# Optimization experiments

Hardware: AMD Instinct MI355X
Metric: run time of the kernel (lower is better)

## Reference

```python
import jax, jax.numpy as jnp
import numpy as np

B, N, C = 32, 2048, 1024  # batch, tokens, embed_dim
LN_EPS = 1e-5


@jax.custom_vjp
def ste(x):
    # StraightThroughEstimator: hard threshold at 0.5
    return (x > 0.5).astype(x.dtype)

def _ste_fwd(x):
    return ste(x), None

def _ste_bwd(res, g):
    # torch backward: F.hardtanh(grad_output) -> clamp grad to [-1, 1]
    return (jnp.clip(g, -1.0, 1.0),)

ste.defvjp(_ste_fwd, _ste_bwd)


def layernorm(x, scale, bias, eps=LN_EPS):
    mu = jnp.mean(x, axis=-1, keepdims=True)
    var = jnp.mean(jnp.square(x - mu), axis=-1, keepdims=True)
    return (x - mu) * jax.lax.rsqrt(var + eps) * scale + bias


def setup_inputs() -> dict:
    key = jax.random.key(0)
    ks = jax.random.split(key, 8)
    u = lambda k, shape, fan_in: jax.random.uniform(
        k, shape, jnp.float32, -1.0 / np.sqrt(fan_in), 1.0 / np.sqrt(fan_in))
    return {
        "input_feature": jax.random.normal(ks[0], (B, N, C), jnp.float32),
        "noise_feature": jax.random.normal(ks[1], (1, 1, C // 2), jnp.float32),
        "prev_m": jnp.ones((B, N), jnp.float32),
        "ln_scale": jnp.ones((C,), jnp.float32),
        "ln_bias": jnp.zeros((C,), jnp.float32),
        "W_L": u(ks[2], (C, C // 2), C),        # norm1 -> L (no bias)
        "W_l1": u(ks[3], (C, C // 2), C),       # cat(C/2, C/2)=C -> C/2
        "W_l2": u(ks[4], (C // 2, C // 4), C // 2),
        "W_l3": u(ks[5], (C // 4, 1), C // 4),
    }


def reference(input_feature, noise_feature, prev_m,
              ln_scale, ln_bias, W_L, W_l1, W_l2, W_l3):
    Bn, Nn, Cd = input_feature.shape
    # gating MLP (chan_mask_gen)
    h = jax.nn.gelu(layernorm(input_feature, ln_scale, ln_bias) @ W_L,
                    approximate=False)                       # [B,N,C/2]
    nf = jnp.broadcast_to(noise_feature, (Bn, Nn, noise_feature.shape[-1]))
    h = jnp.concatenate([h, nf], axis=-1)                    # [B,N,C]
    h = jax.nn.gelu(h @ W_l1, approximate=False)             # [B,N,C/2]
    h = jax.nn.gelu(h @ W_l2, approximate=False)             # [B,N,C/4]
    prob = jax.nn.sigmoid(h @ W_l3)[..., 0]                  # [B,N]

    # training-path chanFSM: STE mask + elementwise gating
    curr_m = ste(prob * prev_m)                              # {0,1} float
    mask = curr_m.astype(jnp.int32)
    out = input_feature * curr_m[..., None]                  # [B,N,C]
    return out, mask, curr_m + 1e-10
```

## Files before the change

kernel.cpp:

```cpp
#include <hip/hip_runtime.h>
#include <hip/hip_bf16.h>
#include <math.h>

#define T_TOK 65536
#define C_DIM 1024
#define H_DIM 512
#define Q_DIM 256

typedef __attribute__((ext_vector_type(8))) _Float16 half8;
typedef __attribute__((ext_vector_type(4))) float f32x4;
typedef unsigned int u32;
typedef unsigned short u16;

#define MFMAF(a, b, c) __builtin_amdgcn_mfma_f32_16x16x32_f16((a), (b), (c), 0, 0, 0)

#define WS_B1H 0u
#define WS_B1L (WS_B1H + 1048576u)
#define WS_B2H (WS_B1L + 1048576u)
#define WS_B2L (WS_B2H + 524288u)
#define WS_B3H (WS_B2L + 524288u)
#define WS_B3L (WS_B3H + 262144u)
#define WS_BIAS2 (WS_B3L + 262144u)
#define WS_CNT  (WS_BIAS2 + 2048u)
#define WS_LIST (WS_CNT + 256u)
#define WS_W3   (WS_LIST + 32768u)
#define WS_NEED (WS_W3 + 1024u)

#define RC_CAP 8192
#define RC_EPS 5e-5f

__device__ __forceinline__ float gelu_exact(float x) {
    return 0.5f * x * (1.0f + erff(x * 0.70710678118654752440f));
}
__device__ __forceinline__ void split_a(float f, u16& hi, u16& lo) {
    _Float16 h = (_Float16)f;
    _Float16 l = (_Float16)((f - (float)h) * 2048.0f);
    hi = __builtin_bit_cast(u16, h);
    lo = __builtin_bit_cast(u16, l);
}
__device__ __forceinline__ void split_w(float f, u16& hi, u16& lo) {
    _Float16 h = (_Float16)f;
    _Float16 l = (_Float16)(f - (float)h);
    hi = __builtin_bit_cast(u16, h);
    lo = __builtin_bit_cast(u16, l);
}
__device__ __forceinline__ float comb(float m, float r) {
    return fmaf(r, 4.8828125e-4f, m) * 0.03125f;
}

__global__ __launch_bounds__(256) void pack_kernel(const float* __restrict__ WL,
                                                   const float* __restrict__ Wl1,
                                                   const float* __restrict__ Wl2,
                                                   const float* __restrict__ w3,
                                                   unsigned char* __restrict__ ws) {
    u16* B1h = (u16*)(ws + WS_B1H); u16* B1l = (u16*)(ws + WS_B1L);
    u16* B2h = (u16*)(ws + WS_B2H); u16* B2l = (u16*)(ws + WS_B2L);
    u16* B3h = (u16*)(ws + WS_B3H); u16* B3l = (u16*)(ws + WS_B3L);
    int gid = blockIdx.x * 256 + threadIdx.x;
    if (gid == 0) *(int*)(ws + WS_CNT) = 0;
    if (gid < 256) ((float*)(ws + WS_W3))[gid] = w3[gid];
    int lane = gid & 63;
    int tg = gid >> 6;
    int kq = lane >> 4;
    int nn = lane & 15;
    if (tg < 1024) {
        int nt = tg >> 5, kt = tg & 31;
        int n = nt * 16 + nn;
        #pragma unroll
        for (int j = 0; j < 8; ++j) {
            int k = kt * 32 + kq * 8 + j;
            u16 h, l; split_w(WL[(size_t)k * 512 + n] * 32.0f, h, l);
            B1h[(size_t)tg * 512 + lane * 8 + j] = h;
            B1l[(size_t)tg * 512 + lane * 8 + j] = l;
        }
    } else if (tg < 1536) {
        int t2 = tg - 1024;
        int nt = t2 >> 4, kt = t2 & 15;
        int n = nt * 16 + nn;
        #pragma unroll
        for (int j = 0; j < 8; ++j) {
            int k = kt * 32 + kq * 8 + j;
            u16 h, l; split_w(Wl1[(size_t)k * 512 + n] * 32.0f, h, l);
            B2h[(size_t)t2 * 512 + lane * 8 + j] = h;
            B2l[(size_t)t2 * 512 + lane * 8 + j] = l;
        }
    } else if (tg < 1792) {
        int t3 = tg - 1536;
        int nt = t3 >> 4, kt = t3 & 15;
        int n = nt * 16 + nn;
        #pragma unroll
        for (int j = 0; j < 8; ++j) {
            int k = kt * 32 + kq * 8 + j;
            u16 h, l; split_w(Wl2[(size_t)k * 256 + n] * 32.0f, h, l);
            B3h[(size_t)t3 * 512 + lane * 8 + j] = h;
            B3l[(size_t)t3 * 512 + lane * 8 + j] = l;
        }
    }
}

__global__ void bias2_kernel(const float* __restrict__ nf,
                             const float* __restrict__ Wl1,
                             float* __restrict__ bias2) {
    int n = blockIdx.x * blockDim.x + threadIdx.x;
    if (n >= H_DIM) return;
    float s = 0.0f;
    for (int j = 0; j < H_DIM; ++j)
        s = fmaf(nf[j], Wl1[(size_t)(H_DIM + j) * H_DIM + n], s);
    bias2[n] = s;
}

#define MTOK 32
#define SA_STR 136
#define SH_STR 520
#define S3_STR 260

__global__ __launch_bounds__(512, 4)
void chanFSM_mfma_kernel(const float* __restrict__ x,
                         const float* __restrict__ prev_m,
                         const float* __restrict__ gamma,
                         const float* __restrict__ beta,
                         const unsigned char* __restrict__ ws,
                         float* __restrict__ out,
                         float* __restrict__ out_mask,
                         float* __restrict__ out_curr) {
    __shared__ __align__(16) unsigned char smem[66560];
    __shared__ float sMu[MTOK], sRs[MTOK], sFlag[MTOK];
    __shared__ float sBias[H_DIM];
    __shared__ float sw3[Q_DIM];

    u16* sAh = (u16*)smem;
    u16* sAl = sAh + MTOK * SA_STR;
    u16* sHh = (u16*)smem;
    u16* sHl = sHh + MTOK * SH_STR;
    float* sH3 = (float*)smem;

    const u16* B1h = (const u16*)(ws + WS_B1H); const u16* B1l = (const u16*)(ws + WS_B1L);
    const u16* B2h = (const u16*)(ws + WS_B2H); const u16* B2l = (const u16*)(ws + WS_B2L);
    const u16* B3h = (const u16*)(ws + WS_B3H); const u16* B3l = (const u16*)(ws + WS_B3L);
    int* rc_cnt  = (int*)(ws + WS_CNT);
    int* rc_list = (int*)(ws + WS_LIST);

    const int tid = threadIdx.x;
    const int t0  = blockIdx.x * MTOK;
    const int wid = tid >> 6;
    const int ln  = tid & 63;
    const int rg  = wid & 1;
    const int cg  = wid >> 1;
    const int lm  = ln & 15;
    const int lq  = ln >> 4;

    if (tid < H_DIM) sBias[tid] = ((const float*)(ws + WS_BIAS2))[tid];
    if (tid < Q_DIM) sw3[tid] = ((const float*)(ws + WS_W3))[tid];

    for (int m = wid * 4; m < wid * 4 + 4; ++m) {
        const float* row = x + (size_t)(t0 + m) * C_DIM;
        double ds = 0.0, dq = 0.0;
        #pragma unroll
        for (int j = 0; j < 16; ++j) {
            float v = row[ln + (j << 6)];
            ds += (double)v; dq += (double)v * (double)v;
        }
        #pragma unroll
        for (int off = 32; off > 0; off >>= 1) {
            ds += __shfl_down(ds, off);
            dq += __shfl_down(dq, off);
        }
        if (ln == 0) {
            double mu = ds * (1.0 / 1024.0);
            double var = dq * (1.0 / 1024.0) - mu * mu;
            sMu[m] = (float)mu;
            sRs[m] = 1.0f / sqrtf((float)var + 1e-5f);
        }
    }

    f32x4 acc_m[8], acc_r[8];
    #pragma unroll
    for (int c = 0; c < 8; ++c) {
        acc_m[c] = (f32x4){0.f, 0.f, 0.f, 0.f};
        acc_r[c] = (f32x4){0.f, 0.f, 0.f, 0.f};
    }

    for (int chunk = 0; chunk < 8; ++chunk) {
        __syncthreads();
        #pragma unroll
        for (int i = 0; i < 2; ++i) {
            int fq = tid + (i << 9);
            int row = fq >> 5, kq = fq & 31;
            const float4 v = *(const float4*)&x[(size_t)(t0 + row) * C_DIM + chunk * 128 + kq * 4];
            float mu = sMu[row], rs = sRs[row];
            int gk = chunk * 128 + kq * 4;
            float a0 = fmaf((v.x - mu) * rs, gamma[gk],     beta[gk]);
            float a1 = fmaf((v.y - mu) * rs, gamma[gk + 1], beta[gk + 1]);
            float a2 = fmaf((v.z - mu) * rs, gamma[gk + 2], beta[gk + 2]);
            float a3 = fmaf((v.w - mu) * rs, gamma[gk + 3], beta[gk + 3]);
            u16 h0, l0, h1, l1, h2, l2, h3, l3;
            split_a(a0, h0, l0); split_a(a1, h1, l1);
            split_a(a2, h2, l2); split_a(a3, h3, l3);
            uint2 ph = make_uint2((u32)h0 | ((u32)h1 << 16), (u32)h2 | ((u32)h3 << 16));
            uint2 pl = make_uint2((u32)l0 | ((u32)l1 << 16), (u32)l2 | ((u32)l3 << 16));
            *(uint2*)&sAh[row * SA_STR + kq * 4] = ph;
            *(uint2*)&sAl[row * SA_STR + kq * 4] = pl;
        }
        __syncthreads();

        #pragma unroll
        for (int kt = 0; kt < 4; ++kt) {
            int row = rg * 16 + lm;
            half8 ah = *(const half8*)&sAh[row * SA_STR + kt * 32 + lq * 8];
            half8 al = *(const half8*)&sAl[row * SA_STR + kt * 32 + lq * 8];
            int ktg = chunk * 4 + kt;
            #pragma unroll
            for (int chf = 0; chf < 2; ++chf) {
                half8 bh[4], bl[4];
                #pragma unroll
                for (int c = 0; c < 4; ++c) {
                    int tile = (cg * 8 + chf * 4 + c) * 32 + ktg;
                    bh[c] = *(const half8*)&B1h[(size_t)tile * 512 + ln * 8];
                    bl[c] = *(const half8*)&B1l[(size_t)tile * 512 + ln * 8];
                }
                #pragma unroll
                for (int c = 0; c < 4; ++c) {
                    int cc = chf * 4 + c;
                    acc_m[cc] = MFMAF(ah, bh[c], acc_m[cc]);
                    acc_m[cc] = MFMAF(ah, bl[c], acc_m[cc]);
                    acc_r[cc] = MFMAF(al, bh[c], acc_r[cc]);
                }
            }
        }
    }
    __syncthreads();
    #pragma unroll
    for (int c = 0; c < 8; ++c) {
        int col = (cg * 8 + c) * 16 + lm;
        #pragma unroll
        for (int r = 0; r < 4; ++r) {
            int row = rg * 16 + lq * 4 + r;
            u16 h, l; split_a(gelu_exact(comb(acc_m[c][r], acc_r[c][r])), h, l);
            sHh[row * SH_STR + col] = h;
            sHl[row * SH_STR + col] = l;
        }
    }
    __syncthreads();

    f32x4 acc2_m[8], acc2_r[8];
    #pragma unroll
    for (int c = 0; c < 8; ++c) {
        float b = sBias[(cg * 8 + c) * 16 + lm] * 32.0f;
        acc2_m[c] = (f32x4){b, b, b, b};
        acc2_r[c] = (f32x4){0.f, 0.f, 0.f, 0.f};
    }
    #pragma unroll 2
    for (int kt = 0; kt < 16; ++kt) {
        int row = rg * 16 + lm;
        half8 ah = *(const half8*)&sHh[row * SH_STR + kt * 32 + lq * 8];
        half8 al = *(const half8*)&sHl[row * SH_STR + kt * 32 + lq * 8];
        #pragma unroll
        for (int chf = 0; chf < 2; ++chf) {
            half8 bh[4], bl[4];
            #pragma unroll
            for (int c = 0; c < 4; ++c) {
                int tile = (cg * 8 + chf * 4 + c) * 16 + kt;
                bh[c] = *(const half8*)&B2h[(size_t)tile * 512 + ln * 8];
                bl[c] = *(const half8*)&B2l[(size_t)tile * 512 + ln * 8];
            }
            #pragma unroll
            for (int c = 0; c < 4; ++c) {
                int cc = chf * 4 + c;
                acc2_m[cc] = MFMAF(ah, bh[c], acc2_m[cc]);
                acc2_m[cc] = MFMAF(ah, bl[c], acc2_m[cc]);
                acc2_r[cc] = MFMAF(al, bh[c], acc2_r[cc]);
            }
        }
    }
    __syncthreads();
    #pragma unroll
    for (int c = 0; c < 8; ++c) {
        int col = (cg * 8 + c) * 16 + lm;
        #pragma unroll
        for (int r = 0; r < 4; ++r) {
            int row = rg * 16 + lq * 4 + r;
            u16 h, l; split_a(gelu_exact(comb(acc2_m[c][r], acc2_r[c][r])), h, l);
            sHh[row * SH_STR + col] = h;
            sHl[row * SH_STR + col] = l;
        }
    }
    __syncthreads();

    f32x4 acc3_m[4], acc3_r[4];
    #pragma unroll
    for (int c = 0; c < 4; ++c) {
        acc3_m[c] = (f32x4){0.f, 0.f, 0.f, 0.f};
        acc3_r[c] = (f32x4){0.f, 0.f, 0.f, 0.f};
    }
    #pragma unroll 2
    for (int kt = 0; kt < 16; ++kt) {
        int row = rg * 16 + lm;
        half8 ah = *(const half8*)&sHh[row * SH_STR + kt * 32 + lq * 8];
        half8 al = *(const half8*)&sHl[row * SH_STR + kt * 32 + lq * 8];
        half8 bh[4], bl[4];
        #pragma unroll
        for (int c = 0; c < 4; ++c) {
            int tile = (cg * 4 + c) * 16 + kt;
            bh[c] = *(const half8*)&B3h[(size_t)tile * 512 + ln * 8];
            bl[c] = *(const half8*)&B3l[(size_t)tile * 512 + ln * 8];
        }
        #pragma unroll
        for (int c = 0; c < 4; ++c) {
            acc3_m[c] = MFMAF(ah, bh[c], acc3_m[c]);
            acc3_m[c] = MFMAF(ah, bl[c], acc3_m[c]);
            acc3_r[c] = MFMAF(al, bh[c], acc3_r[c]);
        }
    }
    __syncthreads();
    #pragma unroll
    for (int c = 0; c < 4; ++c) {
        int col = (cg * 4 + c) * 16 + lm;
        #pragma unroll
        for (int r = 0; r < 4; ++r) {
            int row = rg * 16 + lq * 4 + r;
            sH3[row * S3_STR + col] = gelu_exact(comb(acc3_m[c][r], acc3_r[c][r]));
        }
    }
    __syncthreads();

    for (int m = wid * 4; m < wid * 4 + 4; ++m) {
        float z = 0.0f;
        #pragma unroll
        for (int j = 0; j < 4; ++j) {
            int k = ln + (j << 6);
            z = fmaf(sH3[m * S3_STR + k], sw3[k], z);
        }
        #pragma unroll
        for (int off = 32; off > 0; off >>= 1) z += __shfl_down(z, off);
        if (ln == 0) {
            float prob = 1.0f / (1.0f + expf(-z));
            float t = prob * prev_m[t0 + m];
            float c = (t > 0.5f) ? 1.0f : 0.0f;
            sFlag[m] = c;
            out_mask[t0 + m] = c;
            out_curr[t0 + m] = (c > 0.0f) ? 1.0f : 1e-10f;
            if (fabsf(t - 0.5f) < RC_EPS) {
                int i = atomicAdd(rc_cnt, 1);
                if (i < RC_CAP) rc_list[i] = t0 + m;
            }
        }
    }
    __syncthreads();

    const float4* x4 = (const float4*)(x   + (size_t)t0 * C_DIM);
    float4*       o4 = (float4*)      (out + (size_t)t0 * C_DIM);
    #pragma unroll 4
    for (int i = 0; i < 16; ++i) {
        int idx = tid + (i << 9);
        int m = idx >> 8;
        float c = sFlag[m];
        float4 v = x4[idx];
        v.x *= c; v.y *= c; v.z *= c; v.w *= c;
        o4[idx] = v;
    }
}

__global__ __launch_bounds__(256, 2)
void recheck_kernel(const float* __restrict__ x, const float* __restrict__ prev_m,
                    const float* __restrict__ gamma, const float* __restrict__ beta,
                    const float* __restrict__ WL, const float* __restrict__ Wl1,
                    const float* __restrict__ Wl2, const float* __restrict__ w3,
                    const unsigned char* __restrict__ ws,
                    float* __restrict__ out, float* __restrict__ out_mask,
                    float* __restrict__ out_curr) {
    __shared__ __align__(16) float sx[8 * 1024];
    __shared__ __align__(16) float sh1[8 * 512];
    __shared__ __align__(16) float sh2[8 * 512];
    __shared__ __align__(16) float sh3[8 * 256];
    __shared__ double srA[8][4], srB[8][4];
    __shared__ float sMu[8], sRs[8], sFlag[8];
    __shared__ int sTok[8];

    const float* bias2 = (const float*)(ws + WS_BIAS2);
    const int* cnt = (const int*)(ws + WS_CNT);
    const int* list = (const int*)(ws + WS_LIST);
    int n = *cnt; if (n > RC_CAP) n = RC_CAP;
    if (blockIdx.x * 8 >= n) return;

    const int tid = threadIdx.x, wid = tid >> 6, ln = tid & 63;

    if (tid < 8) {
        int it = blockIdx.x * 8 + tid;
        sTok[tid] = (it < n) ? list[it] : -1;
    }
    __syncthreads();

    #pragma unroll
    for (int g = 0; g < 8; ++g) {
        int tk = sTok[g];
        if (tk >= 0) {
            const float* row = x + (size_t)tk * C_DIM;
            #pragma unroll
            for (int j = 0; j < 4; ++j)
                sx[g * 1024 + tid + (j << 8)] = row[tid + (j << 8)];
        } else {
            #pragma unroll
            for (int j = 0; j < 4; ++j)
                sx[g * 1024 + tid + (j << 8)] = 0.f;
        }
    }
    __syncthreads();

    #pragma unroll
    for (int g = 0; g < 8; ++g) {
        double ds = 0.0, dq = 0.0;
        #pragma unroll
        for (int j = 0; j < 4; ++j) {
            float v = sx[g * 1024 + tid + (j << 8)];
            ds += (double)v; dq += (double)v * (double)v;
        }
        #pragma unroll
        for (int off = 32; off > 0; off >>= 1) {
            ds += __shfl_down(ds, off); dq += __shfl_down(dq, off);
        }
        if (ln == 0) { srA[g][wid] = ds; srB[g][wid] = dq; }
    }
    __syncthreads();
    if (tid < 8) {
        double tds = srA[tid][0] + srA[tid][1] + srA[tid][2] + srA[tid][3];
        double tdq = srB[tid][0] + srB[tid][1] + srB[tid][2] + srB[tid][3];
        double mud = tds * (1.0 / 1024.0);
        sMu[tid] = (float)mud;
        sRs[tid] = 1.0f / sqrtf((float)(tdq * (1.0 / 1024.0) - mud * mud) + 1e-5f);
    }
    __syncthreads();
    #pragma unroll
    for (int g = 0; g < 8; ++g) {
        float mu = sMu[g], rs = sRs[g];
        #pragma unroll
        for (int j = 0; j < 4; ++j) {
            int k = tid + (j << 8);
            sx[g * 1024 + k] = fmaf((sx[g * 1024 + k] - mu) * rs, gamma[k], beta[k]);
        }
    }
    __syncthreads();

    {
        float acc[2][8][4];
        #pragma unroll
        for (int o = 0; o < 2; ++o)
            #pragma unroll
            for (int g = 0; g < 8; ++g)
                #pragma unroll
                for (int i = 0; i < 4; ++i) acc[o][g][i] = 0.f;
        const float2* Wp = (const float2*)WL + tid;
        #pragma unroll 4
        for (int k = 0; k < 1024; k += 4) {
            float2 w0 = Wp[(size_t)(k + 0) * 256];
            float2 w1 = Wp[(size_t)(k + 1) * 256];
            float2 w2 = Wp[(size_t)(k + 2) * 256];
            float2 w3v = Wp[(size_t)(k + 3) * 256];
            #pragma unroll
            for (int g = 0; g < 8; ++g) {
                float4 a = *(const float4*)&sx[g * 1024 + k];
                acc[0][g][0] = fmaf(a.x, w0.x, acc[0][g][0]);
                acc[1][g][0] = fmaf(a.x, w0.y, acc[1][g][0]);
                acc[0][g][1] = fmaf(a.y, w1.x, acc[0][g][1]);
                acc[1][g][1] = fmaf(a.y, w1.y, acc[1][g][1]);
                acc[0][g][2] = fmaf(a.z, w2.x, acc[0][g][2]);
                acc[1][g][2] = fmaf(a.z, w2.y, acc[1][g][2]);
                acc[0][g][3] = fmaf(a.w, w3v.x, acc[0][g][3]);
                acc[1][g][3] = fmaf(a.w, w3v.y, acc[1][g][3]);
            }
        }
        #pragma unroll
        for (int g = 0; g < 8; ++g) {
            float o0 = (acc[0][g][0] + acc[0][g][1]) + (acc[0][g][2] + acc[0][g][3]);
            float o1 = (acc[1][g][0] + acc[1][g][1]) + (acc[1][g][2] + acc[1][g][3]);
            float2 gv; gv.x = gelu_exact(o0); gv.y = gelu_exact(o1);
            *(float2*)&sh1[g * 512 + 2 * tid] = gv;
        }
    }
    __syncthreads();

    {
        float acc[2][8][4];
        float2 b2 = ((const float2*)bias2)[tid];
        #pragma unroll
        for (int g = 0; g < 8; ++g) {
            acc[0][g][0] = b2.x; acc[1][g][0] = b2.y;
            #pragma unroll
            for (int i = 1; i < 4; ++i) { acc[0][g][i] = 0.f; acc[1][g][i] = 0.f; }
        }
        const float2* Wp = (const float2*)Wl1 + tid;
        #pragma unroll 4
        for (int k = 0; k < 512; k += 4) {
            float2 w0 = Wp[(size_t)(k + 0) * 256];
            float2 w1 = Wp[(size_t)(k + 1) * 256];
            float2 w2 = Wp[(size_t)(k + 2) * 256];
            float2 w3v = Wp[(size_t)(k + 3) * 256];
            #pragma unroll
            for (int g = 0; g < 8; ++g) {
                float4 a = *(const float4*)&sh1[g * 512 + k];
                acc[0][g][0] = fmaf(a.x, w0.x, acc[0][g][0]);
                acc[1][g][0] = fmaf(a.x, w0.y, acc[1][g][0]);
                acc[0][g][1] = fmaf(a.y, w1.x, acc[0][g][1]);
                acc[1][g][1] = fmaf(a.y, w1.y, acc[1][g][1]);
                acc[0][g][2] = fmaf(a.z, w2.x, acc[0][g][2]);
                acc[1][g][2] = fmaf(a.z, w2.y, acc[1][g][2]);
                acc[0][g][3] = fmaf(a.w, w3v.x, acc[0][g][3]);
                acc[1][g][3] = fmaf(a.w, w3v.y, acc[1][g][3]);
            }
        }
        #pragma unroll
        for (int g = 0; g < 8; ++g) {
            float o0 = (acc[0][g][0] + acc[0][g][1]) + (acc[0][g][2] + acc[0][g][3]);
            float o1 = (acc[1][g][0] + acc[1][g][1]) + (acc[1][g][2] + acc[1][g][3]);
            float2 gv; gv.x = gelu_exact(o0); gv.y = gelu_exact(o1);
            *(float2*)&sh2[g * 512 + 2 * tid] = gv;
        }
    }
    __syncthreads();

    {
        float acc[8][4];
        #pragma unroll
        for (int g = 0; g < 8; ++g)
            #pragma unroll
            for (int i = 0; i < 4; ++i) acc[g][i] = 0.f;
        const float* Wp = Wl2 + tid;
        #pragma unroll 4
        for (int k = 0; k < 512; k += 4) {
            float w0 = Wp[(size_t)(k + 0) * 256];
            float w1 = Wp[(size_t)(k + 1) * 256];
            float w2 = Wp[(size_t)(k + 2) * 256];
            float w3v = Wp[(size_t)(k + 3) * 256];
            #pragma unroll
            for (int g = 0; g < 8; ++g) {
                float4 a = *(const float4*)&sh2[g * 512 + k];
                acc[g][0] = fmaf(a.x, w0, acc[g][0]);
                acc[g][1] = fmaf(a.y, w1, acc[g][1]);
                acc[g][2] = fmaf(a.z, w2, acc[g][2]);
                acc[g][3] = fmaf(a.w, w3v, acc[g][3]);
            }
        }
        #pragma unroll
        for (int g = 0; g < 8; ++g)
            sh3[g * 256 + tid] = gelu_exact((acc[g][0] + acc[g][1]) + (acc[g][2] + acc[g][3]));
    }
    __syncthreads();

    {
        float zz[8];
        float wv = w3[tid];
        #pragma unroll
        for (int g = 0; g < 8; ++g) zz[g] = sh3[g * 256 + tid] * wv;
        #pragma unroll
        for (int off = 32; off > 0; off >>= 1) {
            #pragma unroll
            for (int g = 0; g < 8; ++g) zz[g] += __shfl_down(zz[g], off);
        }
        if (ln == 0) {
            #pragma unroll
            for (int g = 0; g < 8; ++g) srA[g][wid] = (double)zz[g];
        }
    }
    __syncthreads();
    if (tid < 8) {
        int tk = sTok[tid];
        if (tk >= 0) {
            float z = (float)(srA[tid][0] + srA[tid][1] + srA[tid][2] + srA[tid][3]);
            float prob = 1.0f / (1.0f + expf(-z));
            float t = prob * prev_m[tk];
            float c = (t > 0.5f) ? 1.0f : 0.0f;
            out_mask[tk] = c;
            out_curr[tk] = (c > 0.0f) ? 1.0f : 1e-10f;
            sFlag[tid] = c;
        }
    }
    __syncthreads();
    #pragma unroll
    for (int g = 0; g < 8; ++g) {
        int tk = sTok[g];
        if (tk < 0) continue;
        float c = sFlag[g];
        float4 v = ((const float4*)(x + (size_t)tk * C_DIM))[tid];
        v.x *= c; v.y *= c; v.z *= c; v.w *= c;
        ((float4*)(out + (size_t)tk * C_DIM))[tid] = v;
    }
}

extern "C" void kernel_launch(void* const* d_in, const int* in_sizes, int n_in,
                              void* d_out, int out_size, void* d_ws, size_t ws_size,
                              hipStream_t stream) {
    const float* x      = (const float*)d_in[0];
    const float* nf     = (const float*)d_in[1];
    const float* prev_m = (const float*)d_in[2];
    const float* gamma  = (const float*)d_in[3];
    const float* beta   = (const float*)d_in[4];
    const float* WL     = (const float*)d_in[5];
    const float* Wl1    = (const float*)d_in[6];
    const float* Wl2    = (const float*)d_in[7];
    const float* w3     = (const float*)d_in[8];

    float* out      = (float*)d_out;
    float* out_mask = out + (size_t)T_TOK * C_DIM;
    float* out_curr = out_mask + T_TOK;

    unsigned char* ws = (unsigned char*)d_ws;

    pack_kernel<<<448, 256, 0, stream>>>(WL, Wl1, Wl2, w3, ws);
    bias2_kernel<<<1, 512, 0, stream>>>(nf, Wl1, (float*)(ws + WS_BIAS2));

    chanFSM_mfma_kernel<<<T_TOK / MTOK, 512, 0, stream>>>(
        x, prev_m, gamma, beta, ws, out, out_mask, out_curr);

    recheck_kernel<<<RC_CAP / 8, 256, 0, stream>>>(
        x, prev_m, gamma, beta, WL, Wl1, Wl2, w3, ws, out, out_mask, out_curr);
}
```

Baseline: 1.726 ms.

## Double tile rows per block, double-buffer LN staging, widen recheck kernel

The main MLP kernel now handles 64 tokens per block, with each wave computing two 16-row MFMA tiles, so every weight fragment loaded from global memory is reused twice. The LayerNorm-to-fp16 staging is double-buffered: the next chunk of x is loaded into registers and written to the other LDS buffer while the current one is consumed, which removes one barrier per chunk. The recheck kernel moves to 512 threads processing 16 tokens per block. The cost is roughly doubled LDS use (133KB) and accumulator registers, with launch bounds lowered to 2 blocks, so occupancy and latency hiding may drop.

Result: slower. 1.832 ms (+6.1%).

```diff
diff --git a/kernel.cpp b/kernel.cpp
--- a/kernel.cpp
+++ b/kernel.cpp
@@ -104,17 +104,45 @@
     int n = blockIdx.x * blockDim.x + threadIdx.x;
     if (n >= H_DIM) return;
     float s = 0.0f;
+    #pragma unroll 8
     for (int j = 0; j < H_DIM; ++j)
         s = fmaf(nf[j], Wl1[(size_t)(H_DIM + j) * H_DIM + n], s);
     bias2[n] = s;
 }
 
-#define MTOK 32
+#define MTOK 64
 #define SA_STR 136
 #define SH_STR 520
 #define S3_STR 260
 
-__global__ __launch_bounds__(512, 4)
+__device__ __forceinline__ void stage_proc(u16* __restrict__ dAh, u16* __restrict__ dAl,
+                                           const float4* xv, int tid, int chunk,
+                                           const float* __restrict__ sMu,
+                                           const float* __restrict__ sRs,
+                                           const float* __restrict__ gamma,
+                                           const float* __restrict__ beta) {
+    #pragma unroll
+    for (int i = 0; i < 4; ++i) {
+        int fq = tid + (i << 9);
+        int row = fq >> 5, kq = fq & 31;
+        float mu = sMu[row], rs = sRs[row];
+        int gk = chunk * 128 + kq * 4;
+        float4 v = xv[i];
+        float a0 = fmaf((v.x - mu) * rs, gamma[gk],     beta[gk]);
+        float a1 = fmaf((v.y - mu) * rs, gamma[gk + 1], beta[gk + 1]);
+        float a2 = fmaf((v.z - mu) * rs, gamma[gk + 2], beta[gk + 2]);
+        float a3 = fmaf((v.w - mu) * rs, gamma[gk + 3], beta[gk + 3]);
+        u16 h0, l0, h1, l1, h2, l2, h3, l3;
+        split_a(a0, h0, l0); split_a(a1, h1, l1);
+        split_a(a2, h2, l2); split_a(a3, h3, l3);
+        uint2 ph = make_uint2((u32)h0 | ((u32)h1 << 16), (u32)h2 | ((u32)h3 << 16));
+        uint2 pl = make_uint2((u32)l0 | ((u32)l1 << 16), (u32)l2 | ((u32)l3 << 16));
+        *(uint2*)&dAh[row * SA_STR + kq * 4] = ph;
+        *(uint2*)&dAl[row * SA_STR + kq * 4] = pl;
+    }
+}
+
+__global__ __launch_bounds__(512, 2)
 void chanFSM_mfma_kernel(const float* __restrict__ x,
                          const float* __restrict__ prev_m,
                          const float* __restrict__ gamma,
@@ -123,13 +151,16 @@
                          float* __restrict__ out,
                          float* __restrict__ out_mask,
                          float* __restrict__ out_curr) {
-    __shared__ __align__(16) unsigned char smem[66560];
+    __shared__ __align__(16) unsigned char smem[133120];
     __shared__ float sMu[MTOK], sRs[MTOK], sFlag[MTOK];
     __shared__ float sBias[H_DIM];
     __shared__ float sw3[Q_DIM];
 
-    u16* sAh = (u16*)smem;
-    u16* sAl = sAh + MTOK * SA_STR;
+    u16* sA[4];
+    sA[0] = (u16*)smem;
+    sA[1] = sA[0] + MTOK * SA_STR;
+    sA[2] = sA[1] + MTOK * SA_STR;
+    sA[3] = sA[2] + MTOK * SA_STR;
     u16* sHh = (u16*)smem;
     u16* sHl = sHh + MTOK * SH_STR;
     float* sH3 = (float*)smem;
@@ -152,7 +183,7 @@
     if (tid < H_DIM) sBias[tid] = ((const float*)(ws + WS_BIAS2))[tid];
     if (tid < Q_DIM) sw3[tid] = ((const float*)(ws + WS_W3))[tid];
 
-    for (int m = wid * 4; m < wid * 4 + 4; ++m) {
+    for (int m = wid * 8; m < wid * 8 + 8; ++m) {
         const float* row = x + (size_t)(t0 + m) * C_DIM;
         double ds = 0.0, dq = 0.0;
         #pragma unroll
@@ -173,42 +204,48 @@
         }
     }
 
-    f32x4 acc_m[8], acc_r[8];
-    #pragma unroll
-    for (int c = 0; c < 8; ++c) {
-        acc_m[c] = (f32x4){0.f, 0.f, 0.f, 0.f};
-        acc_r[c] = (f32x4){0.f, 0.f, 0.f, 0.f};
-    }
-
-    for (int chunk = 0; chunk < 8; ++chunk) {
+    f32x4 acc_m[2][8], acc_r[2][8];
+    #pragma unroll
+    for (int rt = 0; rt < 2; ++rt)
+        #pragma unroll
+        for (int c = 0; c < 8; ++c) {
+            acc_m[rt][c] = (f32x4){0.f, 0.f, 0.f, 0.f};
+            acc_r[rt][c] = (f32x4){0.f, 0.f, 0.f, 0.f};
+        }
+
+    float4 xv[4];
+    #pragma unroll
+    for (int i = 0; i < 4; ++i) {
+        int fq = tid + (i << 9);
+        int row = fq >> 5, kq = fq & 31;
+        xv[i] = *(const float4*)&x[(size_t)(t0 + row) * C_DIM + kq * 4];
+    }
+    __syncthreads();
+    stage_proc(sA[0], sA[1], xv, tid, 0, sMu, sRs, gamma, beta);
+
+    for (int ch = 0; ch < 8; ++ch) {
+        if (ch < 7) {
+            #pragma unroll
+            for (int i = 0; i < 4; ++i) {
+                int fq = tid + (i << 9);
+                int row = fq >> 5, kq = fq & 31;
+                xv[i] = *(const float4*)&x[(size_t)(t0 + row) * C_DIM + (ch + 1) * 128 + kq * 4];
+            }
+        }
         __syncthreads();
-        #pragma unroll
-        for (int i = 0; i < 2; ++i) {
-            int fq = tid + (i << 9);
-            int row = fq >> 5, kq = fq & 31;
-            const float4 v = *(const float4*)&x[(size_t)(t0 + row) * C_DIM + chunk * 128 + kq * 4];
-            float mu = sMu[row], rs = sRs[row];
-            int gk = chunk * 128 + kq * 4;
-            float a0 = fmaf((v.x - mu) * rs, gamma[gk],     beta[gk]);
-            float a1 = fmaf((v.y - mu) * rs, gamma[gk + 1], beta[gk + 1]);
-            float a2 = fmaf((v.z - mu) * rs, gamma[gk + 2], beta[gk + 2]);
-            float a3 = fmaf((v.w - mu) * rs, gamma[gk + 3], beta[gk + 3]);
-            u16 h0, l0, h1, l1, h2, l2, h3, l3;
-            split_a(a0, h0, l0); split_a(a1, h1, l1);
-            split_a(a2, h2, l2); split_a(a3, h3, l3);
-            uint2 ph = make_uint2((u32)h0 | ((u32)h1 << 16), (u32)h2 | ((u32)h3 << 16));
-            uint2 pl = make_uint2((u32)l0 | ((u32)l1 << 16), (u32)l2 | ((u32)l3 << 16));
-            *(uint2*)&sAh[row * SA_STR + kq * 4] = ph;
-            *(uint2*)&sAl[row * SA_STR + kq * 4] = pl;
-        }
-        __syncthreads();
+        const u16* pAh = sA[(ch & 1) * 2];
+        const u16* pAl = sA[(ch & 1) * 2 + 1];
 
         #pragma unroll
         for (int kt = 0; kt < 4; ++kt) {
-            int row = rg * 16 + lm;
-            half8 ah = *(const half8*)&sAh[row * SA_STR + kt * 32 + lq * 8];
-            half8 al = *(const half8*)&sAl[row * SA_STR + kt * 32 + lq * 8];
-            int ktg = chunk * 4 + kt;
+            half8 ah[2], al[2];
+            #pragma unroll
+            for (int rt = 0; rt < 2; ++rt) {
+                int row = rg * 32 + rt * 16 + lm;
+                ah[rt] = *(const half8*)&pAh[row * SA_STR + kt * 32 + lq * 8];
+                al[rt] = *(const half8*)&pAl[row * SA_STR + kt * 32 + lq * 8];
+            }
+            int ktg = ch * 4 + kt;
             #pragma unroll
             for (int chf = 0; chf < 2; ++chf) {
                 half8 bh[4], bl[4];
@@ -219,41 +256,54 @@
                     bl[c] = *(const half8*)&B1l[(size_t)tile * 512 + ln * 8];
                 }
                 #pragma unroll
-                for (int c = 0; c < 4; ++c) {
-                    int cc = chf * 4 + c;
-                    acc_m[cc] = MFMAF(ah, bh[c], acc_m[cc]);
-                    acc_m[cc] = MFMAF(ah, bl[c], acc_m[cc]);
-                    acc_r[cc] = MFMAF(al, bh[c], acc_r[cc]);
-                }
-            }
-        }
-    }
-    __syncthreads();
-    #pragma unroll
-    for (int c = 0; c < 8; ++c) {
-        int col = (cg * 8 + c) * 16 + lm;
-        #pragma unroll
-        for (int r = 0; r < 4; ++r) {
-            int row = rg * 16 + lq * 4 + r;
-            u16 h, l; split_a(gelu_exact(comb(acc_m[c][r], acc_r[c][r])), h, l);
-            sHh[row * SH_STR + col] = h;
-            sHl[row * SH_STR + col] = l;
-        }
-    }
-    __syncthreads();
-
-    f32x4 acc2_m[8], acc2_r[8];
-    #pragma unroll
-    for (int c = 0; c < 8; ++c) {
-        float b = sBias[(cg * 8 + c) * 16 + lm] * 32.0f;
-        acc2_m[c] = (f32x4){b, b, b, b};
-        acc2_r[c] = (f32x4){0.f, 0.f, 0.f, 0.f};
-    }
+                for (int c = 0; c < 4; ++c)
+                    #pragma unroll
+                    for (int rt = 0; rt < 2; ++rt) {
+                        int cc = chf * 4 + c;
+                        acc_m[rt][cc] = MFMAF(ah[rt], bh[c], acc_m[rt][cc]);
+                        acc_m[rt][cc] = MFMAF(ah[rt], bl[c], acc_m[rt][cc]);
+                        acc_r[rt][cc] = MFMAF(al[rt], bh[c], acc_r[rt][cc]);
+                    }
+            }
+        }
+        if (ch < 7)
+            stage_proc(sA[((ch + 1) & 1) * 2], sA[((ch + 1) & 1) * 2 + 1],
+                       xv, tid, ch + 1, sMu, sRs, gamma, beta);
+    }
+    __syncthreads();
+    #pragma unroll
+    for (int rt = 0; rt < 2; ++rt)
+        #pragma unroll
+        for (int c = 0; c < 8; ++c) {
+            int col = (cg * 8 + c) * 16 + lm;
+            #pragma unroll
+            for (int r = 0; r < 4; ++r) {
+                int row = rg * 32 + rt * 16 + lq * 4 + r;
+                u16 h, l; split_a(gelu_exact(comb(acc_m[rt][c][r], acc_r[rt][c][r])), h, l);
+                sHh[row * SH_STR + col] = h;
+                sHl[row * SH_STR + col] = l;
+            }
+        }
+    __syncthreads();
+
+    f32x4 acc2_m[2][8], acc2_r[2][8];
+    #pragma unroll
+    for (int rt = 0; rt < 2; ++rt)
+        #pragma unroll
+        for (int c = 0; c < 8; ++c) {
+            float b = sBias[(cg * 8 + c) * 16 + lm] * 32.0f;
+            acc2_m[rt][c] = (f32x4){b, b, b, b};
+            acc2_r[rt][c] = (f32x4){0.f, 0.f, 0.f, 0.f};
+        }
     #pragma unroll 2
     for (int kt = 0; kt < 16; ++kt) {
-        int row = rg * 16 + lm;
-        half8 ah = *(const half8*)&sHh[row * SH_STR + kt * 32 + lq * 8];
-        half8 al = *(const half8*)&sHl[row * SH_STR + kt * 32 + lq * 8];
+        half8 ah[2], al[2];
+        #pragma unroll
+        for (int rt = 0; rt < 2; ++rt) {
+            int row = rg * 32 + rt * 16 + lm;
+            ah[rt] = *(const half8*)&sHh[row * SH_STR + kt * 32 + lq * 8];
+            al[rt] = *(const half8*)&sHl[row * SH_STR + kt * 32 + lq * 8];
+        }
         #pragma unroll
         for (int chf = 0; chf < 2; ++chf) {
             half8 bh[4], bl[4];
@@ -264,39 +314,49 @@
                 bl[c] = *(const half8*)&B2l[(size_t)tile * 512 + ln * 8];
             }
             #pragma unroll
-            for (int c = 0; c < 4; ++c) {
-                int cc = chf * 4 + c;
-                acc2_m[cc] = MFMAF(ah, bh[c], acc2_m[cc]);
-                acc2_m[cc] = MFMAF(ah, bl[c], acc2_m[cc]);
-                acc2_r[cc] = MFMAF(al, bh[c], acc2_r[cc]);
-            }
-        }
-    }
-    __syncthreads();
-    #pragma unroll
-    for (int c = 0; c < 8; ++c) {
-        int col = (cg * 8 + c) * 16 + lm;
-        #pragma unroll
-        for (int r = 0; r < 4; ++r) {
-            int row = rg * 16 + lq * 4 + r;
-            u16 h, l; split_a(gelu_exact(comb(acc2_m[c][r], acc2_r[c][r])), h, l);
-            sHh[row * SH_STR + col] = h;
-            sHl[row * SH_STR + col] = l;
-        }
-    }
-    __syncthreads();
-
-    f32x4 acc3_m[4], acc3_r[4];
-    #pragma unroll
-    for (int c = 0; c < 4; ++c) {
-        acc3_m[c] = (f32x4){0.f, 0.f, 0.f, 0.f};
-        acc3_r[c] = (f32x4){0.f, 0.f, 0.f, 0.f};
-    }
+            for (int c = 0; c < 4; ++c)
+                #pragma unroll
+                for (int rt = 0; rt < 2; ++rt) {
+                    int cc = chf * 4 + c;
+                    acc2_m[rt][cc] = MFMAF(ah[rt], bh[c], acc2_m[rt][cc]);
+                    acc2_m[rt][cc] = MFMAF(ah[rt], bl[c], acc2_m[rt][cc]);
+                    acc2_r[rt][cc] = MFMAF(al[rt], bh[c], acc2_r[rt][cc]);
+                }
+        }
+    }
+    __syncthreads();
+    #pragma unroll
+    for (int rt = 0; rt < 2; ++rt)
+        #pragma unroll
+        for (int c = 0; c < 8; ++c) {
+            int col = (cg * 8 + c) * 16 + lm;
+            #pragma unroll
+            for (int r = 0; r < 4; ++r) {
+                int row = rg * 32 + rt * 16 + lq * 4 + r;
+                u16 h, l; split_a(gelu_exact(comb(acc2_m[rt][c][r], acc2_r[rt][c][r])), h, l);
+                sHh[row * SH_STR + col] = h;
+                sHl[row * SH_STR + col] = l;
+            }
+        }
+    __syncthreads();
+
+    f32x4 acc3_m[2][4], acc3_r[2][4];
+    #pragma unroll
+    for (int rt = 0; rt < 2; ++rt)
+        #pragma unroll
+        for (int c = 0; c < 4; ++c) {
+            acc3_m[rt][c] = (f32x4){0.f, 0.f, 0.f, 0.f};
+            acc3_r[rt][c] = (f32x4){0.f, 0.f, 0.f, 0.f};
+        }
     #pragma unroll 2
     for (int kt = 0; kt < 16; ++kt) {
-        int row = rg * 16 + lm;
-        half8 ah = *(const half8*)&sHh[row * SH_STR + kt * 32 + lq * 8];
-        half8 al = *(const half8*)&sHl[row * SH_STR + kt * 32 + lq * 8];
+        half8 ah[2], al[2];
+        #pragma unroll
+        for (int rt = 0; rt < 2; ++rt) {
+            int row = rg * 32 + rt * 16 + lm;
+            ah[rt] = *(const half8*)&sHh[row * SH_STR + kt * 32 + lq * 8];
+            al[rt] = *(const half8*)&sHl[row * SH_STR + kt * 32 + lq * 8];
+        }
         half8 bh[4], bl[4];
         #pragma unroll
         for (int c = 0; c < 4; ++c) {
@@ -305,25 +365,29 @@
             bl[c] = *(const half8*)&B3l[(size_t)tile * 512 + ln * 8];
         }
         #pragma unroll
+        for (int c = 0; c < 4; ++c)
+            #pragma unroll
+            for (int rt = 0; rt < 2; ++rt) {
+                acc3_m[rt][c] = MFMAF(ah[rt], bh[c], acc3_m[rt][c]);
+                acc3_m[rt][c] = MFMAF(ah[rt], bl[c], acc3_m[rt][c]);
+                acc3_r[rt][c] = MFMAF(al[rt], bh[c], acc3_r[rt][c]);
+            }
+    }
+    __syncthreads();
+    #pragma unroll
+    for (int rt = 0; rt < 2; ++rt)
+        #pragma unroll
         for (int c = 0; c < 4; ++c) {
-            acc3_m[c] = MFMAF(ah, bh[c], acc3_m[c]);
-            acc3_m[c] = MFMAF(ah, bl[c], acc3_m[c]);
-            acc3_r[c] = MFMAF(al, bh[c], acc3_r[c]);
-        }
-    }
-    __syncthreads();
-    #pragma unroll
-    for (int c = 0; c < 4; ++c) {
-        int col = (cg * 4 + c) * 16 + lm;
-        #pragma unroll
-        for (int r = 0; r < 4; ++r) {
-            int row = rg * 16 + lq * 4 + r;
-            sH3[row * S3_STR + col] = gelu_exact(comb(acc3_m[c][r], acc3_r[c][r]));
-        }
-    }
-    __syncthreads();
-
-    for (int m = wid * 4; m < wid * 4 + 4; ++m) {
+            int col = (cg * 4 + c) * 16 + lm;
+            #pragma unroll
+            for (int r = 0; r < 4; ++r) {
+                int row = rg * 32 + rt * 16 + lq * 4 + r;
+                sH3[row * S3_STR + col] = gelu_exact(comb(acc3_m[rt][c][r], acc3_r[rt][c][r]));
+            }
+        }
+    __syncthreads();
+
+    for (int m = wid * 8; m < wid * 8 + 8; ++m) {
         float z = 0.0f;
         #pragma unroll
         for (int j = 0; j < 4; ++j) {
@@ -350,7 +414,7 @@
     const float4* x4 = (const float4*)(x   + (size_t)t0 * C_DIM);
     float4*       o4 = (float4*)      (out + (size_t)t0 * C_DIM);
     #pragma unroll 4
-    for (int i = 0; i < 16; ++i) {
+    for (int i = 0; i < 32; ++i) {
         int idx = tid + (i << 9);
         int m = idx >> 8;
         float c = sFlag[m];
@@ -360,7 +424,7 @@
     }
 }
 
-__global__ __launch_bounds__(256, 2)
+__global__ __launch_bounds__(512)
 void recheck_kernel(const float* __restrict__ x, const float* __restrict__ prev_m,
                     const float* __restrict__ gamma, const float* __restrict__ beta,
                     const float* __restrict__ WL, const float* __restrict__ Wl1,
@@ -368,60 +432,63 @@
                     const unsigned char* __restrict__ ws,
                     float* __restrict__ out, float* __restrict__ out_mask,
                     float* __restrict__ out_curr) {
-    __shared__ __align__(16) float sx[8 * 1024];
-    __shared__ __align__(16) float sh1[8 * 512];
-    __shared__ __align__(16) float sh2[8 * 512];
-    __shared__ __align__(16) float sh3[8 * 256];
-    __shared__ double srA[8][4], srB[8][4];
-    __shared__ float sMu[8], sRs[8], sFlag[8];
-    __shared__ int sTok[8];
+    __shared__ __align__(16) float sx[16 * 1024];
+    __shared__ __align__(16) float sh1[16 * 512];
+    __shared__ __align__(16) float sh2[16 * 512];
+    __shared__ __align__(16) float sh3[16 * 256];
+    __shared__ double srA[16][4], srB[16][4];
+    __shared__ float sMu[16], sRs[16], sFlag[16];
+    __shared__ int sTok[16];
 
     const float* bias2 = (const float*)(ws + WS_BIAS2);
     const int* cnt = (const int*)(ws + WS_CNT);
     const int* list = (const int*)(ws + WS_LIST);
     int n = *cnt; if (n > RC_CAP) n = RC_CAP;
-    if (blockIdx.x * 8 >= n) return;
-
-    const int tid = threadIdx.x, wid = tid >> 6, ln = tid & 63;
-
-    if (tid < 8) {
-        int it = blockIdx.x * 8 + tid;
+    if (blockIdx.x * 16 >= n) return;
+
+    const int tid = threadIdx.x;
+    const int grp = tid >> 8;
+    const int t8  = tid & 255;
+    const int wid8 = t8 >> 6;
+    const int ln  = tid & 63;
+
+    if (tid < 16) {
+        int it = blockIdx.x * 16 + tid;
         sTok[tid] = (it < n) ? list[it] : -1;
     }
     __syncthreads();
 
     #pragma unroll
-    for (int g = 0; g < 8; ++g) {
+    for (int g = 0; g < 16; ++g) {
         int tk = sTok[g];
         if (tk >= 0) {
             const float* row = x + (size_t)tk * C_DIM;
-            #pragma unroll
-            for (int j = 0; j < 4; ++j)
-                sx[g * 1024 + tid + (j << 8)] = row[tid + (j << 8)];
+            sx[g * 1024 + tid]       = row[tid];
+            sx[g * 1024 + tid + 512] = row[tid + 512];
         } else {
-            #pragma unroll
-            for (int j = 0; j < 4; ++j)
-                sx[g * 1024 + tid + (j << 8)] = 0.f;
-        }
-    }
-    __syncthreads();
-
-    #pragma unroll
-    for (int g = 0; g < 8; ++g) {
+            sx[g * 1024 + tid] = 0.f;
+            sx[g * 1024 + tid + 512] = 0.f;
+        }
+    }
+    __syncthreads();
+
+    #pragma unroll
+    for (int gg = 0; gg < 8; ++gg) {
+        int g = grp * 8 + gg;
         double ds = 0.0, dq = 0.0;
         #pragma unroll
         for (int j = 0; j < 4; ++j) {
-            float v = sx[g * 1024 + tid + (j << 8)];
+            float v = sx[g * 1024 + t8 + (j << 8)];
             ds += (double)v; dq += (double)v * (double)v;
         }
         #pragma unroll
         for (int off = 32; off > 0; off >>= 1) {
             ds += __shfl_down(ds, off); dq += __shfl_down(dq, off);
         }
-        if (ln == 0) { srA[g][wid] = ds; srB[g][wid] = dq; }
-    }
-    __syncthreads();
-    if (tid < 8) {
+        if (ln == 0) { srA[g][wid8] = ds; srB[g][wid8] = dq; }
+    }
+    __syncthreads();
+    if (tid < 16) {
         double tds = srA[tid][0] + srA[tid][1] + srA[tid][2] + srA[tid][3];
         double tdq = srB[tid][0] + srB[tid][1] + srB[tid][2] + srB[tid][3];
         double mud = tds * (1.0 / 1024.0);
@@ -430,100 +497,79 @@
     }
     __syncthreads();
     #pragma unroll
-    for (int g = 0; g < 8; ++g) {
+    for (int g = 0; g < 16; ++g) {
         float mu = sMu[g], rs = sRs[g];
-        #pragma unroll
-        for (int j = 0; j < 4; ++j) {
-            int k = tid + (j << 8);
-            sx[g * 1024 + k] = fmaf((sx[g * 1024 + k] - mu) * rs, gamma[k], beta[k]);
-        }
+        int k0 = tid, k1 = tid + 512;
+        sx[g * 1024 + k0] = fmaf((sx[g * 1024 + k0] - mu) * rs, gamma[k0], beta[k0]);
+        sx[g * 1024 + k1] = fmaf((sx[g * 1024 + k1] - mu) * rs, gamma[k1], beta[k1]);
     }
     __syncthreads();
 
     {
-        float acc[2][8][4];
-        #pragma unroll
-        for (int o = 0; o < 2; ++o)
-            #pragma unroll
-            for (int g = 0; g < 8; ++g)
-                #pragma unroll
-                for (int i = 0; i < 4; ++i) acc[o][g][i] = 0.f;
-        const float2* Wp = (const float2*)WL + tid;
+        float acc[16][4];
+        #pragma unroll
+        for (int g = 0; g < 16; ++g)
+            #pragma unroll
+            for (int i = 0; i < 4; ++i) acc[g][i] = 0.f;
+        const float* Wp = WL + tid;
         #pragma unroll 4
         for (int k = 0; k < 1024; k += 4) {
-            float2 w0 = Wp[(size_t)(k + 0) * 256];
-            float2 w1 = Wp[(size_t)(k + 1) * 256];
-            float2 w2 = Wp[(size_t)(k + 2) * 256];
-            float2 w3v = Wp[(size_t)(k + 3) * 256];
-            #pragma unroll
-            for (int g = 0; g < 8; ++g) {
+            float w0 = Wp[(size_t)(k + 0) * 512];
+            float w1 = Wp[(size_t)(k + 1) * 512];
+            float w2 = Wp[(size_t)(k + 2) * 512];
+            float w3v = Wp[(size_t)(k + 3) * 512];
+            #pragma unroll
+            for (int g = 0; g < 16; ++g) {
                 float4 a = *(const float4*)&sx[g * 1024 + k];
-                acc[0][g][0] = fmaf(a.x, w0.x, acc[0][g][0]);
-                acc[1][g][0] = fmaf(a.x, w0.y, acc[1][g][0]);
-                acc[0][g][1] = fmaf(a.y, w1.x, acc[0][g][1]);
-                acc[1][g][1] = fmaf(a.y, w1.y, acc[1][g][1]);
-                acc[0][g][2] = fmaf(a.z, w2.x, acc[0][g][2]);
-                acc[1][g][2] = fmaf(a.z, w2.y, acc[1][g][2]);
-                acc[0][g][3] = fmaf(a.w, w3v.x, acc[0][g][3]);
-                acc[1][g][3] = fmaf(a.w, w3v.y, acc[1][g][3]);
-            }
-        }
-        #pragma unroll
-        for (int g = 0; g < 8; ++g) {
-            float o0 = (acc[0][g][0] + acc[0][g][1]) + (acc[0][g][2] + acc[0][g][3]);
-            float o1 = (acc[1][g][0] + acc[1][g][1]) + (acc[1][g][2] + acc[1][g][3]);
-            float2 gv; gv.x = gelu_exact(o0); gv.y = gelu_exact(o1);
-            *(float2*)&sh1[g * 512 + 2 * tid] = gv;
-        }
+                acc[g][0] = fmaf(a.x, w0, acc[g][0]);
+                acc[g][1] = fmaf(a.y, w1, acc[g][1]);
+                acc[g][2] = fmaf(a.z, w2, acc[g][2]);
+                acc[g][3] = fmaf(a.w, w3v, acc[g][3]);
+            }
+        }
+        #pragma unroll
+        for (int g = 0; g < 16; ++g)
+            sh1[g * 512 + tid] = gelu_exact((acc[g][0] + acc[g][1]) + (acc[g][2] + acc[g][3]));
     }
     __syncthreads();
 
     {
-        float acc[2][8][4];
-        float2 b2 = ((const float2*)bias2)[tid];
-        #pragma unroll
-        for (int g = 0; g < 8; ++g) {
-            acc[0][g][0] = b2.x; acc[1][g][0] = b2.y;
-            #pragma unroll
-            for (int i = 1; i < 4; ++i) { acc[0][g][i] = 0.f; acc[1][g][i] = 0.f; }
-        }
-        const float2* Wp = (const float2*)Wl1 + tid;
+        float acc[16][4];
+        float b2 = bias2[tid];
+        #pragma unroll
+        for (int g = 0; g < 16; ++g) {
+            acc[g][0] = b2;
+            acc[g][1] = 0.f; acc[g][2] = 0.f; acc[g][3] = 0.f;
+        }
+        const float* Wp = Wl1 + tid;
         #pragma unroll 4
         for (int k = 0; k < 512; k += 4) {
-            float2 w0 = Wp[(size_t)(k + 0) * 256];
-            float2 w1 = Wp[(size_t)(k + 1) * 256];
-            float2 w2 = Wp[(size_t)(k + 2) * 256];
-            float2 w3v = Wp[(size_t)(k + 3) * 256];
-            #pragma unroll
-            for (int g = 0; g < 8; ++g) {
+            float w0 = Wp[(size_t)(k + 0) * 512];
+            float w1 = Wp[(size_t)(k + 1) * 512];
+            float w2 = Wp[(size_t)(k + 2) * 512];
+            float w3v = Wp[(size_t)(k + 3) * 512];
+            #pragma unroll
+            for (int g = 0; g < 16; ++g) {
                 float4 a = *(const float4*)&sh1[g * 512 + k];
-                acc[0][g][0] = fmaf(a.x, w0.x, acc[0][g][0]);
-                acc[1][g][0] = fmaf(a.x, w0.y, acc[1][g][0]);
-                acc[0][g][1] = fmaf(a.y, w1.x, acc[0][g][1]);
-                acc[1][g][1] = fmaf(a.y, w1.y, acc[1][g][1]);
-                acc[0][g][2] = fmaf(a.z, w2.x, acc[0][g][2]);
-                acc[1][g][2] = fmaf(a.z, w2.y, acc[1][g][2]);
-                acc[0][g][3] = fmaf(a.w, w3v.x, acc[0][g][3]);
-                acc[1][g][3] = fmaf(a.w, w3v.y, acc[1][g][3]);
-            }
-        }
-        #pragma unroll
-        for (int g = 0; g < 8; ++g) {
-            float o0 = (acc[0][g][0] + acc[0][g][1]) + (acc[0][g][2] + acc[0][g][3]);
-            float o1 = (acc[1][g][0] + acc[1][g][1]) + (acc[1][g][2] + acc[1][g][3]);
-            float2 gv; gv.x = gelu_exact(o0); gv.y = gelu_exact(o1);
-            *(float2*)&sh2[g * 512 + 2 * tid] = gv;
-        }
+                acc[g][0] = fmaf(a.x, w0, acc[g][0]);
+                acc[g][1] = fmaf(a.y, w1, acc[g][1]);
+                acc[g][2] = fmaf(a.z, w2, acc[g][2]);
+                acc[g][3] = fmaf(a.w, w3v, acc[g][3]);
+            }
+        }
+        #pragma unroll
+        for (int g = 0; g < 16; ++g)
+            sh2[g * 512 + tid] = gelu_exact((acc[g][0] + acc[g][1]) + (acc[g][2] + acc[g][3]));
     }
     __syncthreads();
 
     {
         float acc[8][4];
         #pragma unroll
-        for (int g = 0; g < 8; ++g)
-            #pragma unroll
-            for (int i = 0; i < 4; ++i) acc[g][i] = 0.f;
-        const float* Wp = Wl2 + tid;
+        for (int gg = 0; gg < 8; ++gg)
+            #pragma unroll
+            for (int i = 0; i < 4; ++i) acc[gg][i] = 0.f;
+        const float* Wp = Wl2 + t8;
         #pragma unroll 4
         for (int k = 0; k < 512; k += 4) {
             float w0 = Wp[(size_t)(k + 0) * 256];
@@ -531,37 +577,38 @@
             float w2 = Wp[(size_t)(k + 2) * 256];
             float w3v = Wp[(size_t)(k + 3) * 256];
             #pragma unroll
-            for (int g = 0; g < 8; ++g) {
-                float4 a = *(const float4*)&sh2[g * 512 + k];
-                acc[g][0] = fmaf(a.x, w0, acc[g][0]);
-                acc[g][1] = fmaf(a.y, w1, acc[g][1]);
-                acc[g][2] = fmaf(a.z, w2, acc[g][2]);
-                acc[g][3] = fmaf(a.w, w3v, acc[g][3]);
-            }
-        }
-        #pragma unroll
-        for (int g = 0; g < 8; ++g)
-            sh3[g * 256 + tid] = gelu_exact((acc[g][0] + acc[g][1]) + (acc[g][2] + acc[g][3]));
+            for (int gg = 0; gg < 8; ++gg) {
+                float4 a = *(const float4*)&sh2[(grp * 8 + gg) * 512 + k];
+                acc[gg][0] = fmaf(a.x, w0, acc[gg][0]);
+                acc[gg][1] = fmaf(a.y, w1, acc[gg][1]);
+                acc[gg][2] = fmaf(a.z, w2, acc[gg][2]);
+                acc[gg][3] = fmaf(a.w, w3v, acc[gg][3]);
+            }
+        }
+        #pragma unroll
+        for (int gg = 0; gg < 8; ++gg)
+            sh3[(grp * 8 + gg) * 256 + t8] =
+                gelu_exact((acc[gg][0] + acc[gg][1]) + (acc[gg][2] + acc[gg][3]));
     }
     __syncthreads();
 
     {
         float zz[8];
-        float wv = w3[tid];
-        #pragma unroll
-        for (int g = 0; g < 8; ++g) zz[g] = sh3[g * 256 + tid] * wv;
+        float wv = w3[t8];
+        #pragma unroll
+        for (int gg = 0; gg < 8; ++gg) zz[gg] = sh3[(grp * 8 + gg) * 256 + t8] * wv;
         #pragma unroll
         for (int off = 32; off > 0; off >>= 1) {
             #pragma unroll
-            for (int g = 0; g < 8; ++g) zz[g] += __shfl_down(zz[g], off);
+            for (int gg = 0; gg < 8; ++gg) zz[gg] += __shfl_down(zz[gg], off);
         }
         if (ln == 0) {
             #pragma unroll
-            for (int g = 0; g < 8; ++g) srA[g][wid] = (double)zz[g];
-        }
-    }
-    __syncthreads();
-    if (tid < 8) {
+            for (int gg = 0; gg < 8; ++gg) srA[grp * 8 + gg][wid8] = (double)zz[gg];
+        }
+    }
+    __syncthreads();
+    if (tid < 16) {
         int tk = sTok[tid];
         if (tk >= 0) {
             float z = (float)(srA[tid][0] + srA[tid][1] + srA[tid][2] + srA[tid][3]);
@@ -575,13 +622,14 @@
     }
     __syncthreads();
     #pragma unroll
-    for (int g = 0; g < 8; ++g) {
+    for (int gg = 0; gg < 8; ++gg) {
+        int g = grp * 8 + gg;
         int tk = sTok[g];
         if (tk < 0) continue;
         float c = sFlag[g];
-        float4 v = ((const float4*)(x + (size_t)tk * C_DIM))[tid];
+        float4 v = ((const float4*)(x + (size_t)tk * C_DIM))[t8];
         v.x *= c; v.y *= c; v.z *= c; v.w *= c;
-        ((float4*)(out + (size_t)tk * C_DIM))[tid] = v;
+        ((float4*)(out + (size_t)tk * C_DIM))[t8] = v;
     }
 }
 
@@ -610,6 +658,6 @@
     chanFSM_mfma_kernel<<<T_TOK / MTOK, 512, 0, stream>>>(
         x, prev_m, gamma, beta, ws, out, out_mask, out_curr);
 
-    recheck_kernel<<<RC_CAP / 8, 256, 0, stream>>>(
+    recheck_kernel<<<RC_CAP / 16, 512, 0, stream>>>(
         x, prev_m, gamma, beta, WL, Wl1, Wl2, w3, ws, out, out_mask, out_curr);
 }
```
